# Kernel tuning notes

Measured on AMD Instinct MI355X. Metric: run time of the kernel, lower is better.

## Reference

```python
import jax, jax.numpy as jnp
import numpy as np
import math

NEG = -1e32
B, S, D, H, DFF, L = 16, 512, 1024, 8, 4096, 3
DK = D // H


def layernorm(x, g, b, eps=1e-5):
    mu = x.mean(-1, keepdims=True)
    var = ((x - mu) ** 2).mean(-1, keepdims=True)
    return (x - mu) / jnp.sqrt(var + eps) * g + b


def gen_dam(alphas, E, bmask):
    # alphas, E: [H, S, 2]; hard gumbel-softmax with straight-through
    Hh, Ss, _ = alphas.shape
    g = -jnp.log(E + 1e-5)
    y_soft = jax.nn.softmax(alphas + g, axis=-1)  # tau = 1
    idx = jnp.argmax(y_soft, axis=-1)
    y_hard = jax.nn.one_hot(idx, 2, dtype=y_soft.dtype)
    m = y_hard - jax.lax.stop_gradient(y_soft) + y_soft
    m = jnp.broadcast_to(m[:, :, 0:1], (Hh, Ss, Ss))
    m = jnp.triu(m)
    m = jnp.rot90(m, 1, axes=(1, 2))
    i = jnp.arange(Ss)[:, None]
    j = jnp.arange(Ss)[None, :]
    src = jnp.clip(j - i, 0, Ss - 1)
    shifted = m[:, jnp.arange(Ss)[:, None], src]  # mask_tri[:, i, j] = m[:, i, j - i]
    mask_tri = jnp.where(j >= i, shifted, 0.0)
    masks = mask_tri + jnp.swapaxes(jnp.triu(mask_tri, 1), 1, 2)
    masks = jnp.triu(masks, bmask)
    return masks


def attention(q, k, v, src_mask, dam, zero_pad, gammas):
    # q,k,v: [B,H,S,dk]; src_mask: [S,S] bool; dam: [H,S,S] bool
    dk = q.shape[-1]
    Ss = q.shape[2]
    scores = jnp.einsum('bhqd,bhkd->bhqk', q, k) / math.sqrt(dk)
    damb = dam[None]          # [1,H,S,S]
    smb = src_mask[None, None]  # [1,1,S,S]
    # NOTE: faithful to the torch code, where the first masked_fill(mask==0)
    # result is overwritten - only dam masks the first softmax.
    sc = jnp.where(damb, scores, NEG)
    sc = jax.nn.softmax(sc, axis=-1)
    sc = sc * smb.astype(sc.dtype) * damb.astype(sc.dtype)
    distcum = jnp.cumsum(sc, axis=-1)
    disttot = jnp.sum(sc, axis=-1, keepdims=True)
    pos = jnp.abs(jnp.arange(Ss)[None, :] - jnp.arange(Ss)[:, None]).astype(scores.dtype)
    dist = jnp.sqrt(jnp.clip((disttot - distcum) * pos[None, None], 0.0, None))
    dist = jax.lax.stop_gradient(dist)
    gamma = -jax.nn.softplus(gammas)[None]  # [1,H,1,1]
    te = jnp.clip(jnp.exp(dist * gamma), 1e-5, 1e5)
    scores = scores * te
    scores = jnp.where(smb, scores, NEG)
    scores = jnp.where(damb, scores, NEG)
    scores = jax.nn.softmax(scores, axis=-1)
    if zero_pad:
        scores = scores.at[:, :, 0, :].set(0.0)
    return jnp.einsum('bhqk,bhkd->bhqd', scores, v)


def transformer_layer(bmask, query, key, values, apply_pos, p):
    Bb, Ss, Dd = query.shape
    Hh = p['gammas'].shape[0]
    dam = gen_dam(p['alphas'], p['E'], bmask) == 0
    src_mask = jnp.triu(jnp.ones((Ss, Ss), jnp.int32), bmask) == 0
    k = (key @ p['kW'].T + p['kb']).reshape(Bb, Ss, Hh, -1).transpose(0, 2, 1, 3)
    q = (query @ p['kW'].T + p['kb']).reshape(Bb, Ss, Hh, -1).transpose(0, 2, 1, 3)  # kq_same
    v = (values @ p['vW'].T + p['vb']).reshape(Bb, Ss, Hh, -1).transpose(0, 2, 1, 3)
    att = attention(q, k, v, src_mask, dam, bmask == 0, p['gammas'])
    concat = att.transpose(0, 2, 1, 3).reshape(Bb, Ss, Dd)
    q2 = concat @ p['oW'].T + p['ob']
    x = layernorm(query + q2, p['ln1_g'], p['ln1_b'])
    if apply_pos:
        ff = jax.nn.relu(x @ p['w1'].T + p['b1']) @ p['w2'].T + p['b2']
        x = layernorm(x + ff, p['ln2_g'], p['ln2_b'])
    return x


def setup_inputs() -> dict:
    key = jax.random.key(0)
    ks = jax.random.split(key, 16)
    sc = 0.02
    return {
        'q_embed_data': jax.random.normal(ks[0], (B, S, D), jnp.float32),
        'qa_embed_data': jax.random.normal(ks[1], (B, S, D), jnp.float32),
        'kW': sc * jax.random.normal(ks[2], (L, D, D), jnp.float32),
        'kb': jnp.zeros((L, D), jnp.float32),
        'vW': sc * jax.random.normal(ks[3], (L, D, D), jnp.float32),
        'vb': jnp.zeros((L, D), jnp.float32),
        'oW': sc * jax.random.normal(ks[4], (L, D, D), jnp.float32),
        'ob': jnp.zeros((L, D), jnp.float32),
        'gammas': 0.5 * jax.random.normal(ks[5], (L, H, 1, 1), jnp.float32),
        'alphas': 0.001 * jax.random.normal(ks[6], (L, H, S, 2), jnp.float32),
        'ln1_g': jnp.ones((L, D), jnp.float32),
        'ln1_b': jnp.zeros((L, D), jnp.float32),
        'w1': sc * jax.random.normal(ks[7], (L, DFF, D), jnp.float32),
        'b1': jnp.zeros((L, DFF), jnp.float32),
        'w2': sc * jax.random.normal(ks[8], (L, D, DFF), jnp.float32),
        'b2': jnp.zeros((L, D), jnp.float32),
        'ln2_g': jnp.ones((L, D), jnp.float32),
        'ln2_b': jnp.zeros((L, D), jnp.float32),
        'gumbel_E': jax.random.exponential(ks[9], (L, H, S, 2), jnp.float32),
    }


def reference(q_embed_data, qa_embed_data, kW, kb, vW, vb, oW, ob, gammas,
              alphas, ln1_g, ln1_b, w1, b1, w2, b2, ln2_g, ln2_b, gumbel_E):
    def P(l):
        return {'kW': kW[l], 'kb': kb[l], 'vW': vW[l], 'vb': vb[l],
                'oW': oW[l], 'ob': ob[l], 'gammas': gammas[l], 'alphas': alphas[l],
                'ln1_g': ln1_g[l], 'ln1_b': ln1_b[l], 'w1': w1[l], 'b1': b1[l],
                'w2': w2[l], 'b2': b2[l], 'ln2_g': ln2_g[l], 'ln2_b': ln2_b[l],
                'E': gumbel_E[l]}
    # blocks_1: self-attention over answer embedding (mask=1)
    y = transformer_layer(1, qa_embed_data, qa_embed_data, qa_embed_data, True, P(0))
    # blocks_2: self-attn on question emb (no FFN), then cross-attn into y
    x = transformer_layer(1, q_embed_data, q_embed_data, q_embed_data, False, P(1))
    x = transformer_layer(0, x, x, y, True, P(2))
    return x
```

## Files before the change

### kernel.cpp

```cpp
#include <hip/hip_runtime.h>
#include <math.h>

#define NEGV -1e32f

typedef __bf16 bf16_t;
typedef _Float16 f16_t;
typedef __bf16 bf16x8 __attribute__((ext_vector_type(8)));
typedef __bf16 bf16x4 __attribute__((ext_vector_type(4)));
typedef _Float16 f16x8 __attribute__((ext_vector_type(8)));
typedef float floatx4 __attribute__((ext_vector_type(4)));

static __device__ __forceinline__ float fexp(float x) { return __expf(x); }
#if __has_builtin(__builtin_amdgcn_sqrtf)
static __device__ __forceinline__ float fsqrt(float x) { return __builtin_amdgcn_sqrtf(x); }
#else
static __device__ __forceinline__ float fsqrt(float x) { return sqrtf(x); }
#endif
#if __has_builtin(__builtin_amdgcn_rcpf)
static __device__ __forceinline__ float frcp(float x) { return __builtin_amdgcn_rcpf(x); }
#else
static __device__ __forceinline__ float frcp(float x) { return 1.0f / x; }
#endif

static __device__ __forceinline__ float wave_sum(float v) {
#pragma unroll
  for (int d = 32; d > 0; d >>= 1) v += __shfl_xor(v, d, 64);
  return v;
}
static __device__ __forceinline__ float wave_max(float v) {
#pragma unroll
  for (int d = 32; d > 0; d >>= 1) v = fmaxf(v, __shfl_xor(v, d, 64));
  return v;
}

static __device__ __forceinline__ void gl2lds16(const bf16_t* g, bf16_t* l) {
  __builtin_amdgcn_global_load_lds((__attribute__((address_space(1))) void*)(void*)g,
                                   (__attribute__((address_space(3))) void*)l, 16, 0, 0);
}

template <int WM, int WN, int FM, int FN, int BIAS_MODE, bool RELU, int OUT_MODE>
__global__ __launch_bounds__(WM * WN * 64) void gemm_db(
    const bf16_t* __restrict__ A, long lda, long a_so, long a_si,
    const bf16_t* __restrict__ B, long ldb, long b_so, long b_si,
    void* __restrict__ Cv, long ldc, long c_so, long c_si,
    const float* __restrict__ bias, int zdiv, int K, float alpha)
{
  constexpr int THREADS = WM * WN * 64;
  constexpr int BM = WM * FM * 16;
  constexpr int BN = WN * FN * 16;
  constexpr int RR = THREADS / 8;
  constexpr int RA = BM / RR;
  constexpr int RB = BN / RR;
  constexpr int NSTG = RA + RB;
  constexpr int MG = (FM >= 8) ? 2 : 1;
  constexpr int MSUB = FM / MG;
  extern __shared__ bf16_t smem[];
  bf16_t* const Asb = smem;
  bf16_t* const Bsb = smem + 2 * (BM * 64);

  const int tid = threadIdx.x;
  const int wave = tid >> 6;
  const int lane = tid & 63;
  const int wm = wave / WN;
  const int wn = wave % WN;
  const int z = blockIdx.z;
  const long zo = z / zdiv;
  const long zi = z % zdiv;
  A += zo * a_so + zi * a_si;
  B += zo * b_so + zi * b_si;
  const long m0 = (long)blockIdx.x * BM;
  const long n0 = (long)blockIdx.y * BN;

  const int srow = tid >> 3;
  const int scol = ((tid & 7) ^ (srow & 7)) * 8;
  const bf16_t* gA = A + (m0 + srow) * lda + scol;
  const bf16_t* gB = B + (n0 + srow) * ldb + scol;
  const int lofs = wave * 512;

  floatx4 acc[FM][FN] = {};
  const int lr = lane & 15;
  const int kg = lane >> 4;
  const int NT = K >> 6;

  auto stage_round = [&](int q, long ko, int dstbuf) {
    if (q < RA)
      gl2lds16(gA + (long)(q * RR) * lda + ko,
               Asb + dstbuf * (BM * 64) + lofs + q * RR * 64);
    else
      gl2lds16(gB + (long)((q - RA) * RR) * ldb + ko,
               Bsb + dstbuf * (BN * 64) + lofs + (q - RA) * RR * 64);
  };

#pragma unroll
  for (int q = 0; q < NSTG; ++q) stage_round(q, 0, 0);

  for (int t = 0; t < NT; ++t) {
    const int buf = t & 1;
    if (t + 1 < NT) {
      const long ko = (long)(t + 1) * 64;
#pragma unroll
      for (int q = 0; q < NSTG; ++q) stage_round(q, ko, buf ^ 1);
      asm volatile("s_waitcnt vmcnt(%0)" :: "n"(NSTG) : "memory");
    } else {
      asm volatile("s_waitcnt vmcnt(0)" ::: "memory");
    }
    __builtin_amdgcn_s_barrier();
    __builtin_amdgcn_sched_barrier(0);
    const bf16_t* __restrict__ Ab = Asb + buf * (BM * 64);
    const bf16_t* __restrict__ Bb = Bsb + buf * (BN * 64);
#pragma unroll
    for (int h = 0; h < 2; ++h) {
      const int slot = ((h * 4 + kg) ^ (lr & 7)) * 8;
      bf16x8 bfr[FN];
#pragma unroll
      for (int g = 0; g < MG; ++g) {
        bf16x8 af[MSUB];
#pragma unroll
        for (int m = 0; m < MSUB; ++m)
          af[m] = *(const bf16x8*)(Ab + (wm * (FM * 16) + (g * MSUB + m) * 16 + lr) * 64 + slot);
        if (g == 0) {
#pragma unroll
          for (int n = 0; n < FN; ++n)
            bfr[n] = *(const bf16x8*)(Bb + (wn * (FN * 16) + n * 16 + lr) * 64 + slot);
        }
        __builtin_amdgcn_sched_barrier(0);
        __builtin_amdgcn_s_barrier();
        __builtin_amdgcn_sched_barrier(0);
        __builtin_amdgcn_s_setprio(1);
#pragma unroll
        for (int m = 0; m < MSUB; ++m)
#pragma unroll
          for (int n = 0; n < FN; ++n)
            acc[g * MSUB + m][n] =
                __builtin_amdgcn_mfma_f32_16x16x32_bf16(af[m], bfr[n], acc[g * MSUB + m][n], 0, 0, 0);
        __builtin_amdgcn_s_setprio(0);
        __builtin_amdgcn_sched_barrier(0);
        __builtin_amdgcn_s_barrier();
      }
    }
  }

  const long coff = zo * c_so + zi * c_si;
  const int q4 = (lane >> 4) * 4;
#pragma unroll
  for (int m = 0; m < FM; ++m) {
#pragma unroll
    for (int n = 0; n < FN; ++n) {
#pragma unroll
      for (int r = 0; r < 4; ++r) {
        const long row = m0 + wm * (FM * 16) + m * 16 + q4 + r;
        const long col = n0 + wn * (FN * 16) + n * 16 + lr;
        float v = acc[m][n][r] * alpha;
        if (BIAS_MODE == 1) v += bias[col];
        if (BIAS_MODE == 2) v += bias[row];
        if (RELU) v = fmaxf(v, 0.0f);
        const long idx = coff + row * ldc + col;
        if (OUT_MODE == 1)      ((bf16_t*)Cv)[idx] = (bf16_t)v;
        else if (OUT_MODE == 2) ((f16_t*)Cv)[idx]  = (f16_t)v;
        else                    ((float*)Cv)[idx]  = v;
      }
    }
  }
}

__global__ __launch_bounds__(256) void cast_kernel(const float* __restrict__ in,
                                                   bf16_t* __restrict__ out, long n)
{
  const long i = ((long)blockIdx.x * 256 + threadIdx.x) * 4;
  if (i >= n) return;
  const float4 v = *(const float4*)(in + i);
  bf16x4 o;
  o[0] = (bf16_t)v.x; o[1] = (bf16_t)v.y; o[2] = (bf16_t)v.z; o[3] = (bf16_t)v.w;
  *(bf16x4*)(out + i) = o;
}

__global__ void bbit_kernel(const float* __restrict__ alphas, const float* __restrict__ E,
                            int* __restrict__ bbit, int n)
{
  const int i = blockIdx.x * 256 + threadIdx.x;
  if (i >= n) return;
  const float l0 = alphas[2 * i]     - logf(E[2 * i]     + 1e-5f);
  const float l1 = alphas[2 * i + 1] - logf(E[2 * i + 1] + 1e-5f);
  bbit[i] = (l0 >= l1) ? 1 : 0;
}

template <bool XBF>
__global__ __launch_bounds__(256) void ln_kernel(
    const void* __restrict__ Xv, const float* __restrict__ R,
    const float* __restrict__ g, const float* __restrict__ b,
    float* __restrict__ out32, bf16_t* __restrict__ out16)
{
  const long row = blockIdx.x;
  const int t = threadIdx.x;
  float x0, x1, x2, x3;
  if (XBF) {
    const bf16x4 xv = *(const bf16x4*)((const bf16_t*)Xv + row * 1024 + t * 4);
    x0 = (float)xv[0]; x1 = (float)xv[1]; x2 = (float)xv[2]; x3 = (float)xv[3];
  } else {
    const float4 xv = *(const float4*)((const float*)Xv + row * 1024 + t * 4);
    x0 = xv.x; x1 = xv.y; x2 = xv.z; x3 = xv.w;
  }
  const float4 rv = *(const float4*)(R + row * 1024 + t * 4);
  const float v0 = x0 + rv.x, v1 = x1 + rv.y, v2 = x2 + rv.z, v3 = x3 + rv.w;
  float s  = v0 + v1 + v2 + v3;
  float s2 = v0 * v0 + v1 * v1 + v2 * v2 + v3 * v3;
  s = wave_sum(s); s2 = wave_sum(s2);
  __shared__ float red[8];
  const int wv = t >> 6, lane = t & 63;
  if (lane == 0) { red[wv] = s; red[4 + wv] = s2; }
  __syncthreads();
  s  = red[0] + red[1] + red[2] + red[3];
  s2 = red[4] + red[5] + red[6] + red[7];
  const float mu = s * (1.0f / 1024.0f);
  const float var = s2 * (1.0f / 1024.0f) - mu * mu;
  const float rstd = rsqrtf(var + 1e-5f);
  const float4 gv = *(const float4*)(g + t * 4);
  const float4 bv = *(const float4*)(b + t * 4);
  float4 ov;
  ov.x = (v0 - mu) * rstd * gv.x + bv.x;
  ov.y = (v1 - mu) * rstd * gv.y + bv.y;
  ov.z = (v2 - mu) * rstd * gv.z + bv.z;
  ov.w = (v3 - mu) * rstd * gv.w + bv.w;
  if (out32) *(float4*)(out32 + row * 1024 + t * 4) = ov;
  if (out16) {
    bf16x4 oh;
    oh[0] = (bf16_t)ov.x; oh[1] = (bf16_t)ov.y; oh[2] = (bf16_t)ov.z; oh[3] = (bf16_t)ov.w;
    *(bf16x4*)(out16 + row * 1024 + t * 4) = oh;
  }
}

__global__ __launch_bounds__(256) void attn_mid(
    const f16_t* __restrict__ S, bf16_t* __restrict__ P,
    const int* __restrict__ bbit, const float* __restrict__ gam,
    const int bmask, const int zero_pad)
{
  const int wid = threadIdx.x >> 6;
  const int lane = threadIdx.x & 63;
  const long rowid = (long)blockIdx.x * 4 + wid;
  const int i = (int)(rowid & 511);
  const int h = (int)(rowid >> 9) & 7;
  const f16_t* s = S + rowid * 512;
  const int jb = lane * 8;

  const float gv = gam[h];
  const float gamma = -log1pf(fexp(gv));

  float sv[8];
  {
    const f16x8 a = *(const f16x8*)(s + jb);
#pragma unroll
    for (int u = 0; u < 8; ++u) sv[u] = (float)a[u];
  }
  const int* bb = bbit + h * 512;
  float z[8];
  bool band[8];
  float m1 = NEGV;
#pragma unroll
  for (int u = 0; u < 8; ++u) {
    const int j = jb + u;
    const bool bd = j < i + bmask;
    band[u] = bd;
    int d = j - i; d = d < 0 ? 0 : d;
    const bool allowed = bd || (bb[d] == 0);
    z[u] = allowed ? sv[u] : NEGV;
    m1 = fmaxf(m1, z[u]);
  }
  m1 = wave_max(m1);
  float e[8], es = 0.f;
#pragma unroll
  for (int u = 0; u < 8; ++u) { e[u] = fexp(z[u] - m1); es += e[u]; }
  es = wave_sum(es);
  const float inv1 = frcp(es);

  float c[8];
  float run = 0.f;
#pragma unroll
  for (int u = 0; u < 8; ++u) {
    const float p = band[u] ? e[u] * inv1 : 0.f;
    run += p;
    c[u] = run;
  }
  float x = run;
#pragma unroll
  for (int d = 1; d < 64; d <<= 1) {
    const float y = __shfl_up(x, (unsigned)d, 64);
    if (lane >= d) x += y;
  }
  const float tot = __shfl(x, 63, 64);
  const float ex = x - run;

  float z2[8];
  float m2 = NEGV;
#pragma unroll
  for (int u = 0; u < 8; ++u) {
    const int j = jb + u;
    const float cc = c[u] + ex;
    const float pos = fabsf((float)(i - j));
    const float dist = fsqrt(fmaxf((tot - cc) * pos, 0.f));
    float te = fexp(dist * gamma);
    te = fminf(fmaxf(te, 1e-5f), 1e5f);
    z2[u] = band[u] ? sv[u] * te : NEGV;
    m2 = fmaxf(m2, z2[u]);
  }
  m2 = wave_max(m2);
  float f[8], es2 = 0.f;
#pragma unroll
  for (int u = 0; u < 8; ++u) { f[u] = fexp(z2[u] - m2); es2 += f[u]; }
  es2 = wave_sum(es2);
  const float inv2 = (zero_pad && i == 0) ? 0.f : frcp(es2);
  bf16x8 o;
#pragma unroll
  for (int u = 0; u < 8; ++u) o[u] = (bf16_t)(f[u] * inv2);
  *(bf16x8*)(P + rowid * 512 + jb) = o;
}

extern "C" void kernel_launch(void* const* d_in, const int* in_sizes, int n_in,
                              void* d_out, int out_size, void* d_ws, size_t ws_size,
                              hipStream_t stream)
{
  (void)in_sizes; (void)n_in; (void)out_size; (void)ws_size;
  const float* q_emb  = (const float*)d_in[0];
  const float* qa_emb = (const float*)d_in[1];
  const float* kW = (const float*)d_in[2];
  const float* kb = (const float*)d_in[3];
  const float* vW = (const float*)d_in[4];
  const float* vb = (const float*)d_in[5];
  const float* oW = (const float*)d_in[6];
  const float* ob = (const float*)d_in[7];
  const float* gammas = (const float*)d_in[8];
  const float* alphas = (const float*)d_in[9];
  const float* ln1_g = (const float*)d_in[10];
  const float* ln1_b = (const float*)d_in[11];
  const float* w1 = (const float*)d_in[12];
  const float* b1 = (const float*)d_in[13];
  const float* w2 = (const float*)d_in[14];
  const float* b2 = (const float*)d_in[15];
  const float* ln2_g = (const float*)d_in[16];
  const float* ln2_b = (const float*)d_in[17];
  const float* gumE = (const float*)d_in[18];
  float* outp = (float*)d_out;

  static bool attr_done = false;
  if (!attr_done) {
    attr_done = true;
    (void)hipFuncSetAttribute(reinterpret_cast<const void*>(&gemm_db<2,2,4,4,1,false,1>),
                              hipFuncAttributeMaxDynamicSharedMemorySize, 65536);
    (void)hipFuncSetAttribute(reinterpret_cast<const void*>(&gemm_db<2,2,4,4,2,false,1>),
                              hipFuncAttributeMaxDynamicSharedMemorySize, 65536);
    (void)hipFuncSetAttribute(reinterpret_cast<const void*>(&gemm_db<2,2,4,4,0,false,1>),
                              hipFuncAttributeMaxDynamicSharedMemorySize, 65536);
    (void)hipFuncSetAttribute(reinterpret_cast<const void*>(&gemm_db<2,2,4,4,0,false,2>),
                              hipFuncAttributeMaxDynamicSharedMemorySize, 65536);
    (void)hipFuncSetAttribute(reinterpret_cast<const void*>(&gemm_db<2,2,4,4,1,false,0>),
                              hipFuncAttributeMaxDynamicSharedMemorySize, 65536);
    (void)hipFuncSetAttribute(reinterpret_cast<const void*>(&gemm_db<2,4,8,4,1,true,1>),
                              hipFuncAttributeMaxDynamicSharedMemorySize, 131072);
  }

  const size_t MBc = 1ull << 20;
  char* W = (char*)d_ws;
  int*    bbit = (int*)W;
  bf16_t* VB   = (bf16_t*)(W + 1 * MBc);
  bf16_t* XB   = (bf16_t*)(W + 17 * MBc);
  bf16_t* kWb  = (bf16_t*)(W + 33 * MBc);
  bf16_t* vWb  = (bf16_t*)(W + 39 * MBc);
  bf16_t* oWb  = (bf16_t*)(W + 45 * MBc);
  bf16_t* w1b  = (bf16_t*)(W + 51 * MBc);
  bf16_t* w2b  = (bf16_t*)(W + 59 * MBc);
  bf16_t* KQB  = (bf16_t*)(W + 67 * MBc);
  bf16_t* VT   = (bf16_t*)(W + 83 * MBc);
  f16_t*  SSPP = (f16_t*)(W + 99 * MBc);
  bf16_t* PPb  = (bf16_t*)(W + 99 * MBc);
  bf16_t* ATT  = (bf16_t*)(W + 163 * MBc);
  float*  O32  = (float*)(W + 67 * MBc);
  bf16_t* X1B  = (bf16_t*)(W + 99 * MBc);
  bf16_t* H1B  = (bf16_t*)(W + 115 * MBc);

  const long ND = 8388608;

  auto run_layer = [&](int l, const void* Qin, bool qin_bf16, const bf16_t* XBp,
                       const bf16_t* VBp, bool apply_pos, int bmask,
                       float* o32, bf16_t* o16) {
    const bf16_t* kWl = kWb + (long)l * 1048576;
    const bf16_t* vWl = vWb + (long)l * 1048576;
    const bf16_t* oWl = oWb + (long)l * 1048576;
    gemm_db<2,2,4,4,1,false,1><<<dim3(64, 8, 1), dim3(256), 65536, stream>>>(
        XBp, 1024, 0, 0, kWl, 1024, 0, 0, (void*)KQB, 1024, 0, 0,
        kb + l * 1024, 1, 1024, 1.0f);
    gemm_db<2,2,4,4,2,false,1><<<dim3(8, 4, 16), dim3(256), 65536, stream>>>(
        vWl, 1024, 0, 0, VBp, 1024, 524288, 0, (void*)VT, 512, 524288, 0,
        vb + l * 1024, 1, 1024, 1.0f);
    const int zp = (bmask == 0) ? 1 : 0;
    gemm_db<2,2,4,4,0,false,2><<<dim3(4, 4, 128), dim3(256), 65536, stream>>>(
        KQB, 1024, 524288, 128, KQB, 1024, 524288, 128,
        (void*)SSPP, 512, 2097152, 262144, nullptr, 8, 128, 0.08838834764831845f);
    attn_mid<<<dim3(16384), dim3(256), 0, stream>>>(
        SSPP, PPb, bbit + l * 4096, gammas + l * 8, bmask, zp);
    gemm_db<2,2,4,4,0,false,1><<<dim3(4, 1, 128), dim3(256), 65536, stream>>>(
        PPb, 512, 2097152, 262144, VT, 512, 524288, 65536,
        (void*)ATT, 1024, 524288, 128, nullptr, 8, 512, 1.0f);
    gemm_db<2,2,4,4,1,false,0><<<dim3(64, 8, 1), dim3(256), 65536, stream>>>(
        ATT, 1024, 0, 0, oWl, 1024, 0, 0, (void*)O32, 1024, 0, 0,
        ob + l * 1024, 1, 1024, 1.0f);
    if (!apply_pos) {
      if (qin_bf16)
        ln_kernel<true><<<dim3(8192), dim3(256), 0, stream>>>(
            Qin, O32, ln1_g + l * 1024, ln1_b + l * 1024, o32, o16);
      else
        ln_kernel<false><<<dim3(8192), dim3(256), 0, stream>>>(
            Qin, O32, ln1_g + l * 1024, ln1_b + l * 1024, o32, o16);
    } else {
      cast_kernel<<<dim3(4096), dim3(256), 0, stream>>>(w1 + (long)l * 4194304, w1b, 4194304);
      cast_kernel<<<dim3(4096), dim3(256), 0, stream>>>(w2 + (long)l * 4194304, w2b, 4194304);
      if (qin_bf16)
        ln_kernel<true><<<dim3(8192), dim3(256), 0, stream>>>(
            Qin, O32, ln1_g + l * 1024, ln1_b + l * 1024, nullptr, X1B);
      else
        ln_kernel<false><<<dim3(8192), dim3(256), 0, stream>>>(
            Qin, O32, ln1_g + l * 1024, ln1_b + l * 1024, nullptr, X1B);
      gemm_db<2,4,8,4,1,true,1><<<dim3(32, 16, 1), dim3(512), 131072, stream>>>(
          X1B, 1024, 0, 0, w1b, 1024, 0, 0, (void*)H1B, 4096, 0, 0,
          b1 + l * 4096, 1, 1024, 1.0f);
      gemm_db<2,2,4,4,1,false,0><<<dim3(64, 8, 1), dim3(256), 65536, stream>>>(
          H1B, 4096, 0, 0, w2b, 4096, 0, 0, (void*)O32, 1024, 0, 0,
          b2 + l * 1024, 1, 4096, 1.0f);
      ln_kernel<true><<<dim3(8192), dim3(256), 0, stream>>>(
          X1B, O32, ln2_g + l * 1024, ln2_b + l * 1024, o32, o16);
    }
  };

  bbit_kernel<<<dim3(48), dim3(256), 0, stream>>>(alphas, gumE, bbit, 12288);
  cast_kernel<<<dim3(3072), dim3(256), 0, stream>>>(kW, kWb, 3145728);
  cast_kernel<<<dim3(3072), dim3(256), 0, stream>>>(vW, vWb, 3145728);
  cast_kernel<<<dim3(3072), dim3(256), 0, stream>>>(oW, oWb, 3145728);

  cast_kernel<<<dim3(8192), dim3(256), 0, stream>>>(qa_emb, XB, ND);
  run_layer(0, qa_emb, false, XB, XB, true, 1, nullptr, VB);
  cast_kernel<<<dim3(8192), dim3(256), 0, stream>>>(q_emb, XB, ND);
  run_layer(1, q_emb, false, XB, XB, false, 1, nullptr, XB);
  run_layer(2, XB, true, XB, VB, true, 0, outp, nullptr);
}
```

Baseline: 1.125 ms.

## Fuse QK^T, masked double-softmax and PV into one attention kernel; interleave GEMM prefetch

Replaces the three attention launches (score GEMM, row-wise distance-decay softmax, PV GEMM) with one kernel per 32-query block. It keeps the score tile in shared memory, so the f16 score and bf16 probability tensors no longer round-trip through global memory. Separately, the generic GEMM now spreads next-tile global-to-LDS staging across the MFMA phases and drops one barrier per phase. The fused kernel uses about 74KB of LDS and small 32-row tiles, which may lower occupancy and MFMA efficiency. The GEMM staging split hardcodes 2+6 rounds, so it assumes NSTG equals 8.

```diff
diff --git a/kernel.cpp b/kernel.cpp
--- a/kernel.cpp
+++ b/kernel.cpp
@@ -54,6 +54,7 @@
   constexpr int NSTG = RA + RB;
   constexpr int MG = (FM >= 8) ? 2 : 1;
   constexpr int MSUB = FM / MG;
+  constexpr int PH = 2 * MG;
   extern __shared__ bf16_t smem[];
   bf16_t* const Asb = smem;
   bf16_t* const Bsb = smem + 2 * (BM * 64);
@@ -96,11 +97,12 @@
 
   for (int t = 0; t < NT; ++t) {
     const int buf = t & 1;
-    if (t + 1 < NT) {
-      const long ko = (long)(t + 1) * 64;
-#pragma unroll
-      for (int q = 0; q < NSTG; ++q) stage_round(q, ko, buf ^ 1);
-      asm volatile("s_waitcnt vmcnt(%0)" :: "n"(NSTG) : "memory");
+    const bool pf = (t + 1 < NT);
+    const long ko = (long)(t + 1) * 64;
+    if (pf) {
+#pragma unroll
+      for (int q = 0; q < 2; ++q) stage_round(q, ko, buf ^ 1);
+      asm volatile("s_waitcnt vmcnt(2)" ::: "memory");
     } else {
       asm volatile("s_waitcnt vmcnt(0)" ::: "memory");
     }
@@ -114,6 +116,7 @@
       bf16x8 bfr[FN];
 #pragma unroll
       for (int g = 0; g < MG; ++g) {
+        const int pi = h * MG + g;
         bf16x8 af[MSUB];
 #pragma unroll
         for (int m = 0; m < MSUB; ++m)
@@ -123,8 +126,13 @@
           for (int n = 0; n < FN; ++n)
             bfr[n] = *(const bf16x8*)(Bb + (wn * (FN * 16) + n * 16 + lr) * 64 + slot);
         }
-        __builtin_amdgcn_sched_barrier(0);
-        __builtin_amdgcn_s_barrier();
+        if (pf) {
+          const int q0 = 2 + pi * 6 / PH;
+          const int q1 = 2 + (pi + 1) * 6 / PH;
+#pragma unroll
+          for (int q = q0; q < q1; ++q) stage_round(q, ko, buf ^ 1);
+        }
+        asm volatile("s_waitcnt lgkmcnt(0)" ::: "memory");
         __builtin_amdgcn_sched_barrier(0);
         __builtin_amdgcn_s_setprio(1);
 #pragma unroll
@@ -161,6 +169,219 @@
       }
     }
   }
+}
+
+__global__ __launch_bounds__(256) void attn_fused(
+    const bf16_t* __restrict__ KQ,
+    const bf16_t* __restrict__ VT,
+    bf16_t* __restrict__ ATT,
+    const int* __restrict__ bbit_l, const float* __restrict__ gam,
+    const int bmask, const int zero_pad)
+{
+  extern __shared__ char sm[];
+  f16_t*  Sp16 = (f16_t*)sm;
+  bf16_t* SpB  = (bf16_t*)sm;
+  bf16_t* AQ   = (bf16_t*)(sm + 33280);
+  bf16_t* Bst  = (bf16_t*)(sm + 41472);
+
+  const int tid = threadIdx.x;
+  const int wave = tid >> 6;
+  const int lane = tid & 63;
+  const int lr = lane & 15;
+  const int kg = lane >> 4;
+  const int id = blockIdx.x;
+  const int wg = (id & 7) * 256 + (id >> 3);
+  const int bh = wg >> 4;
+  const int qb = wg & 15;
+  const int b = bh >> 3, h = bh & 7;
+  const bf16_t* Qp = KQ + (long)b * 524288 + h * 128 + (long)qb * 32 * 1024;
+  const bf16_t* Kp = KQ + (long)b * 524288 + h * 128;
+  const bf16_t* Vp = VT + (long)b * 524288 + (long)h * 65536;
+
+  const int srow = tid >> 3;
+  const int scol = ((tid & 7) ^ (srow & 7)) * 8;
+  const int lofs = wave * 512;
+
+  gl2lds16(Qp + (long)srow * 1024 + scol,       AQ + lofs);
+  gl2lds16(Qp + (long)srow * 1024 + 64 + scol,  AQ + 2048 + lofs);
+#pragma unroll
+  for (int r8 = 0; r8 < 8; ++r8)
+    gl2lds16(Kp + (long)(r8 * 32 + srow) * 1024 + scol, Bst + r8 * 2048 + lofs);
+  __syncthreads();
+
+  floatx4 acc[2][8] = {};
+#pragma unroll
+  for (int step = 0; step < 4; ++step) {
+    const int kt = step >> 1;
+    const int hb = step & 1;
+#pragma unroll
+    for (int hh = 0; hh < 2; ++hh) {
+      const int slot = ((hh * 4 + kg) ^ (lr & 7)) * 8;
+      bf16x8 af[2], bfr[4];
+#pragma unroll
+      for (int m = 0; m < 2; ++m)
+        af[m] = *(const bf16x8*)(AQ + kt * 2048 + (m * 16 + lr) * 64 + slot);
+#pragma unroll
+      for (int n = 0; n < 4; ++n)
+        bfr[n] = *(const bf16x8*)(Bst + (wave * 64 + n * 16 + lr) * 64 + slot);
+#pragma unroll
+      for (int m = 0; m < 2; ++m)
+#pragma unroll
+        for (int n = 0; n < 4; ++n)
+          acc[m][hb * 4 + n] =
+              __builtin_amdgcn_mfma_f32_16x16x32_bf16(af[m], bfr[n], acc[m][hb * 4 + n], 0, 0, 0);
+    }
+    __syncthreads();
+    if (step < 3) {
+      const int kt2 = (step + 1) >> 1;
+      const int hb2 = (step + 1) & 1;
+#pragma unroll
+      for (int r8 = 0; r8 < 8; ++r8)
+        gl2lds16(Kp + (long)(hb2 * 256 + r8 * 32 + srow) * 1024 + kt2 * 64 + scol,
+                 Bst + r8 * 2048 + lofs);
+      __syncthreads();
+    }
+  }
+
+  const int q4 = (lane >> 4) * 4;
+#pragma unroll
+  for (int m = 0; m < 2; ++m)
+#pragma unroll
+    for (int na = 0; na < 8; ++na)
+#pragma unroll
+      for (int rr = 0; rr < 4; ++rr) {
+        const int row = m * 16 + q4 + rr;
+        const int col = (na >> 2) * 256 + wave * 64 + (na & 3) * 16 + lr;
+        Sp16[row * 520 + col] = (f16_t)(acc[m][na][rr] * 0.08838834764831845f);
+      }
+  __syncthreads();
+
+#pragma unroll
+  for (int r3 = 0; r3 < 4; ++r3)
+    gl2lds16(Vp + (long)(r3 * 32 + srow) * 512 + scol, Bst + r3 * 2048 + lofs);
+
+  {
+    const float gamma = -log1pf(fexp(gam[h]));
+    const int* bb = bbit_l + h * 512;
+    const int jb = lane * 8;
+#pragma unroll 1
+    for (int rr8 = 0; rr8 < 8; ++rr8) {
+      const int r = wave * 8 + rr8;
+      const int i = qb * 32 + r;
+      float sv[8];
+      {
+        const f16x8 a = *(const f16x8*)(Sp16 + r * 520 + jb);
+#pragma unroll
+        for (int u = 0; u < 8; ++u) sv[u] = (float)a[u];
+      }
+      float zz[8];
+      bool band[8];
+      float m1 = NEGV;
+#pragma unroll
+      for (int u = 0; u < 8; ++u) {
+        const int j = jb + u;
+        const bool bd = j < i + bmask;
+        band[u] = bd;
+        int d = j - i; d = d < 0 ? 0 : d;
+        const bool allowed = bd || (bb[d] == 0);
+        zz[u] = allowed ? sv[u] : NEGV;
+        m1 = fmaxf(m1, zz[u]);
+      }
+      m1 = wave_max(m1);
+      float e[8], es = 0.f;
+#pragma unroll
+      for (int u = 0; u < 8; ++u) { e[u] = fexp(zz[u] - m1); es += e[u]; }
+      es = wave_sum(es);
+      const float inv1 = frcp(es);
+      float c[8];
+      float run = 0.f;
+#pragma unroll
+      for (int u = 0; u < 8; ++u) {
+        const float p = band[u] ? e[u] * inv1 : 0.f;
+        run += p;
+        c[u] = run;
+      }
+      float x = run;
+#pragma unroll
+      for (int d = 1; d < 64; d <<= 1) {
+        const float y = __shfl_up(x, (unsigned)d, 64);
+        if (lane >= d) x += y;
+      }
+      const float tot = __shfl(x, 63, 64);
+      const float ex = x - run;
+      float z2[8];
+      float m2 = NEGV;
+#pragma unroll
+      for (int u = 0; u < 8; ++u) {
+        const int j = jb + u;
+        const float cc = c[u] + ex;
+        const float pos = fabsf((float)(i - j));
+        const float dist = fsqrt(fmaxf((tot - cc) * pos, 0.f));
+        float te = fexp(dist * gamma);
+        te = fminf(fmaxf(te, 1e-5f), 1e5f);
+        z2[u] = band[u] ? sv[u] * te : NEGV;
+        m2 = fmaxf(m2, z2[u]);
+      }
+      m2 = wave_max(m2);
+      float f[8], es2 = 0.f;
+#pragma unroll
+      for (int u = 0; u < 8; ++u) { f[u] = fexp(z2[u] - m2); es2 += f[u]; }
+      es2 = wave_sum(es2);
+      const float inv2 = (zero_pad && i == 0) ? 0.f : frcp(es2);
+      bf16x8 o;
+#pragma unroll
+      for (int u = 0; u < 8; ++u) o[u] = (bf16_t)(f[u] * inv2);
+      *(bf16x8*)(SpB + r * 520 + jb) = o;
+    }
+  }
+  __syncthreads();
+
+  floatx4 acc2[2][2] = {};
+  for (int kt = 0; kt < 8; ++kt) {
+    const int buf = kt & 1;
+    if (kt < 7) {
+#pragma unroll
+      for (int r3 = 0; r3 < 4; ++r3)
+        gl2lds16(Vp + (long)(r3 * 32 + srow) * 512 + (kt + 1) * 64 + scol,
+                 Bst + (buf ^ 1) * 8192 + r3 * 2048 + lofs);
+      asm volatile("s_waitcnt vmcnt(4)" ::: "memory");
+    } else {
+      asm volatile("s_waitcnt vmcnt(0)" ::: "memory");
+    }
+    __builtin_amdgcn_s_barrier();
+    __builtin_amdgcn_sched_barrier(0);
+#pragma unroll
+    for (int hh = 0; hh < 2; ++hh) {
+      const int ks = hh * 4 + kg;
+      bf16x8 af[2], bfr[2];
+#pragma unroll
+      for (int m = 0; m < 2; ++m)
+        af[m] = *(const bf16x8*)(SpB + (m * 16 + lr) * 520 + kt * 64 + ks * 8);
+#pragma unroll
+      for (int n = 0; n < 2; ++n)
+        bfr[n] = *(const bf16x8*)(Bst + buf * 8192 + (wave * 32 + n * 16 + lr) * 64 +
+                                  (ks ^ (lr & 7)) * 8);
+#pragma unroll
+      for (int m = 0; m < 2; ++m)
+#pragma unroll
+        for (int n = 0; n < 2; ++n)
+          acc2[m][n] = __builtin_amdgcn_mfma_f32_16x16x32_bf16(af[m], bfr[n], acc2[m][n], 0, 0, 0);
+    }
+    __builtin_amdgcn_sched_barrier(0);
+    __builtin_amdgcn_s_barrier();
+  }
+
+#pragma unroll
+  for (int m = 0; m < 2; ++m)
+#pragma unroll
+    for (int n = 0; n < 2; ++n)
+#pragma unroll
+      for (int rr = 0; rr < 4; ++rr) {
+        const int row = m * 16 + q4 + rr;
+        const int col = wave * 32 + n * 16 + lr;
+        ATT[(long)b * 524288 + (long)(qb * 32 + row) * 1024 + h * 128 + col] =
+            (bf16_t)acc2[m][n][rr];
+      }
 }
 
 __global__ __launch_bounds__(256) void cast_kernel(const float* __restrict__ in,
@@ -229,91 +450,6 @@
   }
 }
 
-__global__ __launch_bounds__(256) void attn_mid(
-    const f16_t* __restrict__ S, bf16_t* __restrict__ P,
-    const int* __restrict__ bbit, const float* __restrict__ gam,
-    const int bmask, const int zero_pad)
-{
-  const int wid = threadIdx.x >> 6;
-  const int lane = threadIdx.x & 63;
-  const long rowid = (long)blockIdx.x * 4 + wid;
-  const int i = (int)(rowid & 511);
-  const int h = (int)(rowid >> 9) & 7;
-  const f16_t* s = S + rowid * 512;
-  const int jb = lane * 8;
-
-  const float gv = gam[h];
-  const float gamma = -log1pf(fexp(gv));
-
-  float sv[8];
-  {
-    const f16x8 a = *(const f16x8*)(s + jb);
-#pragma unroll
-    for (int u = 0; u < 8; ++u) sv[u] = (float)a[u];
-  }
-  const int* bb = bbit + h * 512;
-  float z[8];
-  bool band[8];
-  float m1 = NEGV;
-#pragma unroll
-  for (int u = 0; u < 8; ++u) {
-    const int j = jb + u;
-    const bool bd = j < i + bmask;
-    band[u] = bd;
-    int d = j - i; d = d < 0 ? 0 : d;
-    const bool allowed = bd || (bb[d] == 0);
-    z[u] = allowed ? sv[u] : NEGV;
-    m1 = fmaxf(m1, z[u]);
-  }
-  m1 = wave_max(m1);
-  float e[8], es = 0.f;
-#pragma unroll
-  for (int u = 0; u < 8; ++u) { e[u] = fexp(z[u] - m1); es += e[u]; }
-  es = wave_sum(es);
-  const float inv1 = frcp(es);
-
-  float c[8];
-  float run = 0.f;
-#pragma unroll
-  for (int u = 0; u < 8; ++u) {
-    const float p = band[u] ? e[u] * inv1 : 0.f;
-    run += p;
-    c[u] = run;
-  }
-  float x = run;
-#pragma unroll
-  for (int d = 1; d < 64; d <<= 1) {
-    const float y = __shfl_up(x, (unsigned)d, 64);
-    if (lane >= d) x += y;
-  }
-  const float tot = __shfl(x, 63, 64);
-  const float ex = x - run;
-
-  float z2[8];
-  float m2 = NEGV;
-#pragma unroll
-  for (int u = 0; u < 8; ++u) {
-    const int j = jb + u;
-    const float cc = c[u] + ex;
-    const float pos = fabsf((float)(i - j));
-    const float dist = fsqrt(fmaxf((tot - cc) * pos, 0.f));
-    float te = fexp(dist * gamma);
-    te = fminf(fmaxf(te, 1e-5f), 1e5f);
-    z2[u] = band[u] ? sv[u] * te : NEGV;
-    m2 = fmaxf(m2, z2[u]);
-  }
-  m2 = wave_max(m2);
-  float f[8], es2 = 0.f;
-#pragma unroll
-  for (int u = 0; u < 8; ++u) { f[u] = fexp(z2[u] - m2); es2 += f[u]; }
-  es2 = wave_sum(es2);
-  const float inv2 = (zero_pad && i == 0) ? 0.f : frcp(es2);
-  bf16x8 o;
-#pragma unroll
-  for (int u = 0; u < 8; ++u) o[u] = (bf16_t)(f[u] * inv2);
-  *(bf16x8*)(P + rowid * 512 + jb) = o;
-}
-
 extern "C" void kernel_launch(void* const* d_in, const int* in_sizes, int n_in,
                               void* d_out, int out_size, void* d_ws, size_t ws_size,
                               hipStream_t stream)
@@ -347,14 +483,12 @@
                               hipFuncAttributeMaxDynamicSharedMemorySize, 65536);
     (void)hipFuncSetAttribute(reinterpret_cast<const void*>(&gemm_db<2,2,4,4,2,false,1>),
                               hipFuncAttributeMaxDynamicSharedMemorySize, 65536);
-    (void)hipFuncSetAttribute(reinterpret_cast<const void*>(&gemm_db<2,2,4,4,0,false,1>),
-                              hipFuncAttributeMaxDynamicSharedMemorySize, 65536);
-    (void)hipFuncSetAttribute(reinterpret_cast<const void*>(&gemm_db<2,2,4,4,0,false,2>),
-                              hipFuncAttributeMaxDynamicSharedMemorySize, 65536);
     (void)hipFuncSetAttribute(reinterpret_cast<const void*>(&gemm_db<2,2,4,4,1,false,0>),
                               hipFuncAttributeMaxDynamicSharedMemorySize, 65536);
     (void)hipFuncSetAttribute(reinterpret_cast<const void*>(&gemm_db<2,4,8,4,1,true,1>),
                               hipFuncAttributeMaxDynamicSharedMemorySize, 131072);
+    (void)hipFuncSetAttribute(reinterpret_cast<const void*>(&attn_fused),
+                              hipFuncAttributeMaxDynamicSharedMemorySize, 74240);
   }
 
   const size_t MBc = 1ull << 20;
@@ -369,8 +503,6 @@
   bf16_t* w2b  = (bf16_t*)(W + 59 * MBc);
   bf16_t* KQB  = (bf16_t*)(W + 67 * MBc);
   bf16_t* VT   = (bf16_t*)(W + 83 * MBc);
-  f16_t*  SSPP = (f16_t*)(W + 99 * MBc);
-  bf16_t* PPb  = (bf16_t*)(W + 99 * MBc);
   bf16_t* ATT  = (bf16_t*)(W + 163 * MBc);
   float*  O32  = (float*)(W + 67 * MBc);
   bf16_t* X1B  = (bf16_t*)(W + 99 * MBc);
@@ -391,14 +523,8 @@
         vWl, 1024, 0, 0, VBp, 1024, 524288, 0, (void*)VT, 512, 524288, 0,
         vb + l * 1024, 1, 1024, 1.0f);
     const int zp = (bmask == 0) ? 1 : 0;
-    gemm_db<2,2,4,4,0,false,2><<<dim3(4, 4, 128), dim3(256), 65536, stream>>>(
-        KQB, 1024, 524288, 128, KQB, 1024, 524288, 128,
-        (void*)SSPP, 512, 2097152, 262144, nullptr, 8, 128, 0.08838834764831845f);
-    attn_mid<<<dim3(16384), dim3(256), 0, stream>>>(
-        SSPP, PPb, bbit + l * 4096, gammas + l * 8, bmask, zp);
-    gemm_db<2,2,4,4,0,false,1><<<dim3(4, 1, 128), dim3(256), 65536, stream>>>(
-        PPb, 512, 2097152, 262144, VT, 512, 524288, 65536,
-        (void*)ATT, 1024, 524288, 128, nullptr, 8, 512, 1.0f);
+    attn_fused<<<dim3(2048), dim3(256), 74240, stream>>>(
+        KQB, VT, ATT, bbit + l * 4096, gammas + l * 8, bmask, zp);
     gemm_db<2,2,4,4,1,false,0><<<dim3(64, 8, 1), dim3(256), 65536, stream>>>(
         ATT, 1024, 0, 0, oWl, 1024, 0, 0, (void*)O32, 1024, 0, 0,
         ob + l * 1024, 1, 1024, 1.0f);
```

After: 1.177 ms. +4.6%, slower.
